# Performance work log

Hardware: AMD Instinct MI355X
Metric: run time of the kernel (lower is better)

Reference implementation:

```python
import jax, jax.numpy as jnp
import numpy as np

EPS = 1e-7  # K.epsilon()


def setup_inputs() -> dict:
    key = jax.random.key(0)
    k1, k2 = jax.random.split(key)
    B, T, D = 64, 4096, 256
    x = jax.random.normal(k1, (B, T, D), dtype=jnp.float32)
    W = jax.random.normal(k2, (D,), dtype=jnp.float32)
    b = jnp.zeros((T,), dtype=jnp.float32)
    return {"x": x, "W": W, "b": b}


def reference(x, W, b):
    # scores: [B, T] = x . W + b, then tanh
    eij = jnp.tanh(jnp.einsum('btd,d->bt', x, W) + b)
    a = jnp.exp(eij)
    a = a / (jnp.sum(a, axis=1, keepdims=True) + EPS)
    # weighted sum pooling over time: [B, D]
    return jnp.einsum('btd,bt->bd', x, a)
```

## Files before the change

### kernel.cpp

```cpp
#include <hip/hip_runtime.h>
#include <math.h>

#define B_  64
#define T_  4096
#define D_  256
#define BLOCKS_PER_B 32
#define T_PER_BLOCK  (T_ / BLOCKS_PER_B)
#define WAVES_       4
#define T_PER_WAVE   (T_PER_BLOCK / WAVES_)
#define ROWS 4
#define EPS 1e-7f

typedef float vfloat4 __attribute__((ext_vector_type(4)));

__device__ __forceinline__ float exp_tanh(float s) {
    float u = __expf(2.0f * s);
    float t = 1.0f - 2.0f * __builtin_amdgcn_rcpf(u + 1.0f);
    return __expf(t);
}

__global__ __launch_bounds__(256, 4) void attn_pass1(
        const float* __restrict__ x,
        const float* __restrict__ W,
        const float* __restrict__ bias,
        float* __restrict__ partial) {
    const int blk  = blockIdx.x;
    const int b    = blk / BLOCKS_PER_B;
    const int tb   = blk % BLOCKS_PER_B;
    const int wave = threadIdx.x >> 6;
    const int lane = threadIdx.x & 63;
    const int t0   = tb * T_PER_BLOCK + wave * T_PER_WAVE;

    const vfloat4 wv = reinterpret_cast<const vfloat4*>(W)[lane];

    vfloat4 acc = (vfloat4)(0.f);
    float   S   = 0.f;

    const vfloat4* xp = reinterpret_cast<const vfloat4*>(
        x + (size_t)b * T_ * D_ + (size_t)t0 * D_) + lane;

    const int  res  = lane & 3;
    const int  base = lane & ~3;
    const bool o1   = lane & 1;
    const bool o2   = lane & 2;

    #pragma unroll 1
    for (int i = 0; i < T_PER_WAVE; i += ROWS) {
        vfloat4 xv0 = xp[0 * (D_ / 4)];
        vfloat4 xv1 = xp[1 * (D_ / 4)];
        vfloat4 xv2 = xp[2 * (D_ / 4)];
        vfloat4 xv3 = xp[3 * (D_ / 4)];
        xp += ROWS * (D_ / 4);

        float d0 = fmaf(xv0.x, wv.x, fmaf(xv0.y, wv.y, fmaf(xv0.z, wv.z, xv0.w * wv.w)));
        float d1 = fmaf(xv1.x, wv.x, fmaf(xv1.y, wv.y, fmaf(xv1.z, wv.z, xv1.w * wv.w)));
        float d2 = fmaf(xv2.x, wv.x, fmaf(xv2.y, wv.y, fmaf(xv2.z, wv.z, xv2.w * wv.w)));
        float d3 = fmaf(xv3.x, wv.x, fmaf(xv3.y, wv.y, fmaf(xv3.z, wv.z, xv3.w * wv.w)));

        float p  = o1 ? d1 : d0;
        float ps = o1 ? d0 : d1;
        p += __shfl_xor(ps, 1, 64);
        float r  = o1 ? d3 : d2;
        float rs = o1 ? d2 : d3;
        r += __shfl_xor(rs, 1, 64);
        float u  = o2 ? r : p;
        float us = o2 ? p : r;
        u += __shfl_xor(us, 2, 64);
        u += __shfl_xor(u, 4, 64);
        u += __shfl_xor(u, 8, 64);
        u += __shfl_xor(u, 16, 64);
        u += __shfl_xor(u, 32, 64);

        const int t = t0 + i;
        float a_mine = exp_tanh(u + bias[t + res]);
        float a0 = __shfl(a_mine, base + 0, 64);
        float a1 = __shfl(a_mine, base + 1, 64);
        float a2 = __shfl(a_mine, base + 2, 64);
        float a3 = __shfl(a_mine, base + 3, 64);

        acc.x += a0 * xv0.x + a1 * xv1.x + a2 * xv2.x + a3 * xv3.x;
        acc.y += a0 * xv0.y + a1 * xv1.y + a2 * xv2.y + a3 * xv3.y;
        acc.z += a0 * xv0.z + a1 * xv1.z + a2 * xv2.z + a3 * xv3.z;
        acc.w += a0 * xv0.w + a1 * xv1.w + a2 * xv2.w + a3 * xv3.w;
        S += a0 + a1 + a2 + a3;
    }

    __shared__ float sacc[WAVES_][D_];
    __shared__ float sS[WAVES_];
    reinterpret_cast<vfloat4*>(&sacc[wave][0])[lane] = acc;
    if (lane == 0) sS[wave] = S;
    __syncthreads();

    const int d = threadIdx.x;
    float v = sacc[0][d] + sacc[1][d] + sacc[2][d] + sacc[3][d];
    float* p = partial + (size_t)blk * (D_ + 1);
    p[d] = v;
    if (d == 0) p[D_] = sS[0] + sS[1] + sS[2] + sS[3];
}

__global__ __launch_bounds__(256) void attn_pass2(
        const float* __restrict__ partial,
        float* __restrict__ out) {
    const int b = blockIdx.x;
    const int d = threadIdx.x;
    float acc = 0.f, S = 0.f;
    #pragma unroll
    for (int k = 0; k < BLOCKS_PER_B; ++k) {
        const float* p = partial + (size_t)(b * BLOCKS_PER_B + k) * (D_ + 1);
        acc += p[d];
        S   += p[D_];
    }
    out[b * D_ + d] = acc / (S + EPS);
}

extern "C" void kernel_launch(void* const* d_in, const int* in_sizes, int n_in,
                              void* d_out, int out_size, void* d_ws, size_t ws_size,
                              hipStream_t stream) {
    const float* x    = (const float*)d_in[0];
    const float* W    = (const float*)d_in[1];
    const float* bias = (const float*)d_in[2];
    float* out = (float*)d_out;
    float* partial = (float*)d_ws;

    attn_pass1<<<B_ * BLOCKS_PER_B, 256, 0, stream>>>(x, W, bias, partial);
    attn_pass2<<<B_, 256, 0, stream>>>(partial, out);
}
```

Before: 357.5 us.

## Double-buffer x row loads with nontemporal loads in pass1 loop

Restructures the pass1 time loop into a two-stage software pipeline: the next group of four rows is loaded into registers while the current group is reduced and accumulated. Loads use nontemporal hints since x is streamed once, and the occupancy hint in launch bounds is dropped to give the compiler more registers for the extra buffered data. The aim is to hide global memory latency in this bandwidth-bound streaming kernel, at the cost of more register pressure and possibly fewer resident waves.

Measured after the change: 335.4 us. -6.2%, faster.

```diff
diff --git a/kernel.cpp b/kernel.cpp
--- a/kernel.cpp
+++ b/kernel.cpp
@@ -9,6 +9,8 @@
 #define WAVES_       4
 #define T_PER_WAVE   (T_PER_BLOCK / WAVES_)
 #define ROWS 4
+#define ITERS (T_PER_WAVE / ROWS)
+#define GSTRIDE (ROWS * D_ / 4)
 #define EPS 1e-7f
 
 typedef float vfloat4 __attribute__((ext_vector_type(4)));
@@ -19,7 +21,7 @@
     return __expf(t);
 }
 
-__global__ __launch_bounds__(256, 4) void attn_pass1(
+__global__ __launch_bounds__(256) void attn_pass1(
         const float* __restrict__ x,
         const float* __restrict__ W,
         const float* __restrict__ bias,
@@ -44,14 +46,7 @@
     const bool o1   = lane & 1;
     const bool o2   = lane & 2;
 
-    #pragma unroll 1
-    for (int i = 0; i < T_PER_WAVE; i += ROWS) {
-        vfloat4 xv0 = xp[0 * (D_ / 4)];
-        vfloat4 xv1 = xp[1 * (D_ / 4)];
-        vfloat4 xv2 = xp[2 * (D_ / 4)];
-        vfloat4 xv3 = xp[3 * (D_ / 4)];
-        xp += ROWS * (D_ / 4);
-
+    auto consume = [&](vfloat4 xv0, vfloat4 xv1, vfloat4 xv2, vfloat4 xv3, int t) {
         float d0 = fmaf(xv0.x, wv.x, fmaf(xv0.y, wv.y, fmaf(xv0.z, wv.z, xv0.w * wv.w)));
         float d1 = fmaf(xv1.x, wv.x, fmaf(xv1.y, wv.y, fmaf(xv1.z, wv.z, xv1.w * wv.w)));
         float d2 = fmaf(xv2.x, wv.x, fmaf(xv2.y, wv.y, fmaf(xv2.z, wv.z, xv2.w * wv.w)));
@@ -71,7 +66,6 @@
         u += __shfl_xor(u, 16, 64);
         u += __shfl_xor(u, 32, 64);
 
-        const int t = t0 + i;
         float a_mine = exp_tanh(u + bias[t + res]);
         float a0 = __shfl(a_mine, base + 0, 64);
         float a1 = __shfl(a_mine, base + 1, 64);
@@ -83,6 +77,33 @@
         acc.z += a0 * xv0.z + a1 * xv1.z + a2 * xv2.z + a3 * xv3.z;
         acc.w += a0 * xv0.w + a1 * xv1.w + a2 * xv2.w + a3 * xv3.w;
         S += a0 + a1 + a2 + a3;
+    };
+
+    vfloat4 a0 = __builtin_nontemporal_load(&xp[0 * (D_ / 4)]);
+    vfloat4 a1 = __builtin_nontemporal_load(&xp[1 * (D_ / 4)]);
+    vfloat4 a2 = __builtin_nontemporal_load(&xp[2 * (D_ / 4)]);
+    vfloat4 a3 = __builtin_nontemporal_load(&xp[3 * (D_ / 4)]);
+    xp += GSTRIDE;
+
+    #pragma unroll 1
+    for (int i = 0; i < ITERS; i += 2) {
+        vfloat4 b0 = __builtin_nontemporal_load(&xp[0 * (D_ / 4)]);
+        vfloat4 b1 = __builtin_nontemporal_load(&xp[1 * (D_ / 4)]);
+        vfloat4 b2 = __builtin_nontemporal_load(&xp[2 * (D_ / 4)]);
+        vfloat4 b3 = __builtin_nontemporal_load(&xp[3 * (D_ / 4)]);
+        xp += GSTRIDE;
+
+        consume(a0, a1, a2, a3, t0 + i * ROWS);
+
+        if (i + 2 < ITERS) {
+            a0 = __builtin_nontemporal_load(&xp[0 * (D_ / 4)]);
+            a1 = __builtin_nontemporal_load(&xp[1 * (D_ / 4)]);
+            a2 = __builtin_nontemporal_load(&xp[2 * (D_ / 4)]);
+            a3 = __builtin_nontemporal_load(&xp[3 * (D_ / 4)]);
+            xp += GSTRIDE;
+        }
+
+        consume(b0, b1, b2, b3, t0 + (i + 1) * ROWS);
     }
 
     __shared__ float sacc[WAVES_][D_];
@@ -93,9 +114,9 @@
 
     const int d = threadIdx.x;
     float v = sacc[0][d] + sacc[1][d] + sacc[2][d] + sacc[3][d];
-    float* p = partial + (size_t)blk * (D_ + 1);
-    p[d] = v;
-    if (d == 0) p[D_] = sS[0] + sS[1] + sS[2] + sS[3];
+    float* pt = partial + (size_t)blk * (D_ + 1);
+    pt[d] = v;
+    if (d == 0) pt[D_] = sS[0] + sS[1] + sS[2] + sS[3];
 }
 
 __global__ __launch_bounds__(256) void attn_pass2(
```
